# Kernel tuning notes

Measured on AMD Instinct MI355X. Metric: run time of the kernel, lower is better.

Reference implementation:

```python
import jax, jax.numpy as jnp
import numpy as np

NG = 8       # GroupNorm groups
EPS = 1e-5   # torch default eps for GroupNorm/BatchNorm
M_AND = 5    # Anderson history size
MAX_ITER = 25
LAM = 1e-4
BETA = 1.0


def conv2d(x, w):
    # x: [B,C,H,W], w: [O,I,3,3], stride 1, SAME padding (pad=1)
    return jax.lax.conv_general_dilated(x, w, (1, 1), 'SAME',
                                        dimension_numbers=('NCHW', 'OIHW', 'NCHW'))


def group_norm(x, g, b):
    B, C, H, W = x.shape
    xg = x.reshape(B, NG, C // NG, H, W)
    mu = xg.mean((2, 3, 4), keepdims=True)
    var = xg.var((2, 3, 4), keepdims=True)
    xn = ((xg - mu) * jax.lax.rsqrt(var + EPS)).reshape(B, C, H, W)
    return xn * g[None, :, None, None] + b[None, :, None, None]


def batch_norm(x, g, b):
    # training-mode BatchNorm2d: batch statistics over (B,H,W)
    mu = x.mean((0, 2, 3), keepdims=True)
    var = x.var((0, 2, 3), keepdims=True)
    return (x - mu) * jax.lax.rsqrt(var + EPS) * g[None, :, None, None] + b[None, :, None, None]


def resnet_f(p, z, x):
    # y = norm1(relu(conv1(z))); out = norm3(relu(z + norm2(x + conv2(y))))
    y = group_norm(jax.nn.relu(conv2d(z, p['conv1_w'])), p['gn1_g'], p['gn1_b'])
    return group_norm(jax.nn.relu(z + group_norm(x + conv2d(y, p['conv2_w']),
                                                 p['gn2_g'], p['gn2_b'])),
                      p['gn3_g'], p['gn3_b'])


def anderson(f, x0, m=M_AND, lam=LAM, max_iter=MAX_ITER, beta=BETA):
    # Anderson acceleration for fixed point z = f(z); fixed iteration count
    # (the torch version early-exits at tol=0.01; we run the full max_iter for
    # a deterministic jit-friendly reference).
    shape = x0.shape
    bsz = shape[0]
    flat = lambda v: v.reshape(bsz, -1)
    X = [None] * m
    Fv = [None] * m
    X[0] = flat(x0)
    Fv[0] = flat(f(x0))
    X[1] = Fv[0]
    Fv[1] = flat(f(Fv[0].reshape(shape)))
    for k in range(2, max_iter):
        n = min(k, m)
        Xn = jnp.stack(X[:n], 1)   # [B,n,D]
        Fn = jnp.stack(Fv[:n], 1)  # [B,n,D]
        G = Fn - Xn
        Hm = jnp.einsum('bnd,bmd->bnm', G, G) + lam * jnp.eye(n, dtype=x0.dtype)
        Hb = (jnp.zeros((bsz, n + 1, n + 1), x0.dtype)
              .at[:, 1:, 1:].set(Hm)
              .at[:, 0, 1:].set(1.0)
              .at[:, 1:, 0].set(1.0))
        y = jnp.zeros((bsz, n + 1), x0.dtype).at[:, 0].set(1.0)
        alpha = jnp.linalg.solve(Hb, y[..., None])[:, 1:, 0]  # [B,n]
        xk = beta * jnp.einsum('bn,bnd->bd', alpha, Fn) + (1.0 - beta) * jnp.einsum('bn,bnd->bd', alpha, Xn)
        X[k % m] = xk
        Fv[k % m] = flat(f(xk.reshape(shape)))
    return X[(max_iter - 1) % m].reshape(shape)


def setup_inputs() -> dict:
    key = jax.random.key(0)
    ks = jax.random.split(key, 6)
    B, H, W = 8, 128, 200
    f32 = jnp.float32
    return {
        'x': jax.random.normal(ks[0], (B, 1, H, W), f32),
        'conv0_w': jax.random.normal(ks[1], (48, 1, 3, 3), f32) * 0.1,
        'conv0_b': jnp.zeros((48,), f32),
        'bn_g': jnp.ones((48,), f32),
        'bn_b': jnp.zeros((48,), f32),
        'conv1_w': jax.random.normal(ks[2], (64, 48, 3, 3), f32) * 0.01,
        'conv2_w': jax.random.normal(ks[3], (48, 64, 3, 3), f32) * 0.01,
        'gn1_g': jnp.ones((64,), f32), 'gn1_b': jnp.zeros((64,), f32),
        'gn2_g': jnp.ones((48,), f32), 'gn2_b': jnp.zeros((48,), f32),
        'gn3_g': jnp.ones((48,), f32), 'gn3_b': jnp.zeros((48,), f32),
        'fc_w': jax.random.normal(ks[4], (10, 200), f32) * 0.05,
        'fc_b': jnp.zeros((10,), f32),
    }


def reference(x, conv0_w, conv0_b, bn_g, bn_b, conv1_w, conv2_w,
              gn1_g, gn1_b, gn2_g, gn2_b, gn3_g, gn3_b, fc_w, fc_b):
    fp = {'conv1_w': conv1_w, 'conv2_w': conv2_w,
          'gn1_g': gn1_g, 'gn1_b': gn1_b,
          'gn2_g': gn2_g, 'gn2_b': gn2_b,
          'gn3_g': gn3_g, 'gn3_b': gn3_b}
    h = batch_norm(conv2d(x, conv0_w) + conv0_b[None, :, None, None], bn_g, bn_b)
    z_star = anderson(lambda z: resnet_f(fp, z, h), jnp.zeros_like(h))
    z = resnet_f(fp, z_star, h)  # one extra application, as in DEQFixedPoint
    # Linear(200,10) acts on last dim: [B,48,H,200] -> [B,48,H,10]
    return jnp.einsum('bchw,ow->bcho', z, fc_w) + fc_b
```

## Files before the change

kernel.cpp:

```cpp
#include <hip/hip_runtime.h>

#define BB   8
#define HH   128
#define WW   200
#define HWSZ 25600
#define C48  48
#define C64  64
#define NGRP 8
#define EPSV 1e-5f
#define LAMV 1e-4
#define SLOT 9830400
#define DPB  1228800
#define Y64SZ 13107200
#define BIGELEMS 131072000ull

typedef unsigned short bf16_t;
typedef __attribute__((ext_vector_type(4))) short s4v;
typedef __attribute__((ext_vector_type(8))) short s8v;
typedef __attribute__((ext_vector_type(16))) float f32x16;

__device__ inline float b2f(bf16_t b) { return __uint_as_float(((unsigned)b) << 16); }
__device__ inline bf16_t f2b(float f) {
    unsigned u = __float_as_uint(f);
    unsigned r = u + 0x7fffu + ((u >> 16) & 1u);
    return (bf16_t)(r >> 16);
}
__device__ inline float lo16(unsigned u) { return __uint_as_float(u << 16); }
__device__ inline float hi16(unsigned u) { return __uint_as_float(u & 0xffff0000u); }
__device__ inline unsigned pack2(float lo, float hi) {
    return ((unsigned)f2b(lo)) | (((unsigned)f2b(hi)) << 16);
}
__device__ inline float4 ld4(const bf16_t* p) {
    ushort4 u = *(const ushort4*)p;
    return make_float4(b2f(u.x), b2f(u.y), b2f(u.z), b2f(u.w));
}
__device__ inline void st4(bf16_t* p, float4 v) {
    ushort4 u; u.x = f2b(v.x); u.y = f2b(v.y); u.z = f2b(v.z); u.w = f2b(v.w);
    *(ushort4*)p = u;
}
__device__ inline void ld8(const bf16_t* p, float* v) {
    uint4 u = *(const uint4*)p;
    v[0] = lo16(u.x); v[1] = hi16(u.x); v[2] = lo16(u.y); v[3] = hi16(u.y);
    v[4] = lo16(u.z); v[5] = hi16(u.z); v[6] = lo16(u.w); v[7] = hi16(u.w);
}
__device__ inline void st8(bf16_t* p, const float* v) {
    uint4 u;
    u.x = pack2(v[0], v[1]); u.y = pack2(v[2], v[3]);
    u.z = pack2(v[4], v[5]); u.w = pack2(v[6], v[7]);
    *(uint4*)p = u;
}

__device__ inline void ms_from(const double* __restrict__ ds, int pair, double invcnt,
                               float& mean, float& inv) {
    double s = ds[2 * pair], q = ds[2 * pair + 1];
    double m = s * invcnt;
    double v = q * invcnt - m * m;
    mean = (float)m;
    inv = (float)(1.0 / sqrt(v + (double)EPSV));
}


__global__ void zero_kernel(float* __restrict__ p, int n) {
    int i = blockIdx.x * 256 + threadIdx.x;
    if (i < n) p[i] = 0.f;
}
__global__ void fill16_kernel(float4* __restrict__ p) {
    float4 z; z.x = z.y = z.z = z.w = 0.f;
    p[(size_t)blockIdx.x * 256 + threadIdx.x] = z;
}
__global__ void copy16_kernel(float4* __restrict__ dst, const float4* __restrict__ src) {
    size_t i = (size_t)blockIdx.x * 256 + threadIdx.x;
    dst[i] = src[i];
}

__global__ void pack_kernel(const float* __restrict__ w, bf16_t* __restrict__ apk,
                            int CIN, int CO_real, int total) {
    int idx = blockIdx.x * 256 + threadIdx.x;
    if (idx >= total) return;
    int j   = idx & 7;
    int l   = (idx >> 3) & 63;
    int mt  = (idx >> 9) & 1;
    int tap = (idx >> 10) % 9;
    int kc  = idx / 9216;
    int co = mt * 32 + (l & 31);
    int ci = kc * 16 + (l >> 5) * 8 + j;
    float v = (co < CO_real) ? w[((size_t)co * CIN + ci) * 9 + tap] : 0.f;
    apk[idx] = f2b(v);
}

__global__ __launch_bounds__(256) void conv0_kernel(
    const float* __restrict__ x, const float* __restrict__ w0,
    const float* __restrict__ b0, float* __restrict__ out)
{
    __shared__ float xs[3 * 202];
    __shared__ float wt[480];
    const int tid = threadIdx.x;
    const int bI = blockIdx.x / HH, y = blockIdx.x % HH;
    for (int i = tid; i < 606; i += 256) {
        int r = i / 202, cc = i % 202;
        int gy = y + r - 1, gx = cc - 1;
        float v = 0.f;
        if ((unsigned)gy < (unsigned)HH && (unsigned)gx < (unsigned)WW)
            v = x[(size_t)bI * HWSZ + gy * WW + gx];
        xs[r * 202 + cc] = v;
    }
    for (int i = tid; i < 480; i += 256) wt[i] = (i < 432) ? w0[i] : b0[i - 432];
    __syncthreads();
    const size_t obase = (((size_t)bI * HH + y) * WW) * 48;
    for (int ch = tid; ch < 2400; ch += 256) {
        int px = (ch * 4) / 48, c0 = (ch * 4) % 48;
        float xv[3][3];
        #pragma unroll
        for (int r = 0; r < 3; r++)
            #pragma unroll
            for (int dx = 0; dx < 3; dx++)
                xv[r][dx] = xs[r * 202 + px + dx];
        float4 o;
        #pragma unroll
        for (int j = 0; j < 4; j++) {
            int c = c0 + j;
            float acc = wt[432 + c];
            #pragma unroll
            for (int r = 0; r < 3; r++)
                #pragma unroll
                for (int dx = 0; dx < 3; dx++)
                    acc = fmaf(xv[r][dx], wt[c * 9 + r * 3 + dx], acc);
            ((float*)&o)[j] = acc;
        }
        *(float4*)(out + obase + ch * 4) = o;
    }
}

__global__ void bn_stats_kernel(const float* __restrict__ src, double* __restrict__ dst)
{
    __shared__ float ss[192], qq[192];
    const int tid = threadIdx.x;
    const int c = tid % 48, r = tid / 48;
    const int b = blockIdx.y;
    const size_t base = ((size_t)b * HWSZ + (size_t)blockIdx.x * 256) * 48 + c;
    float s = 0.f, q = 0.f;
    for (int p = r; p < 256; p += 4) {
        float v = src[base + (size_t)p * 48];
        s += v; q += v * v;
    }
    ss[tid] = s; qq[tid] = q;
    __syncthreads();
    if (tid < 48) {
        s = ss[tid] + ss[tid + 48] + ss[tid + 96] + ss[tid + 144];
        q = qq[tid] + qq[tid + 48] + qq[tid + 96] + qq[tid + 144];
        unsafeAtomicAdd(&dst[tid * 2],     (double)s);
        unsafeAtomicAdd(&dst[tid * 2 + 1], (double)q);
    }
}

__global__ __launch_bounds__(256) void bn_apply_kernel(
    const float* __restrict__ src, bf16_t* __restrict__ dst,
    const float* __restrict__ gamma, const float* __restrict__ beta,
    const double* __restrict__ ds)
{
    __shared__ float gaT[48], beT[48];
    int tid = threadIdx.x;
    if (tid < 48) {
        float mean, inv; ms_from(ds, tid, 1.0 / 204800.0, mean, inv);
        float ga = gamma[tid] * inv;
        gaT[tid] = ga; beT[tid] = beta[tid] - mean * ga;
    }
    __syncthreads();
    size_t base = (size_t)blockIdx.x * 1024 + (size_t)tid * 4;
    int c0 = (int)(base % 48);
    float4 v = *(const float4*)(src + base);
    ushort4 o;
    o.x = f2b(fmaf(v.x, gaT[c0],     beT[c0]));
    o.y = f2b(fmaf(v.y, gaT[c0 + 1], beT[c0 + 1]));
    o.z = f2b(fmaf(v.z, gaT[c0 + 2], beT[c0 + 2]));
    o.w = f2b(fmaf(v.w, gaT[c0 + 3], beT[c0 + 3]));
    *(ushort4*)(dst + base) = o;
}

template<int CIN, int CIPAD, int CO, int OTS, int CG, bool RELU, bool ADDH, bool FOLDGN>
__global__ __launch_bounds__(256) void conv_mfma_kernel(
    const bf16_t* __restrict__ in, const s8v* __restrict__ apk,
    const bf16_t* __restrict__ hadd, bf16_t* __restrict__ out,
    double* __restrict__ dsOut,
    const double* __restrict__ dsPrev, const float* __restrict__ gPrev,
    const float* __restrict__ bPrev)
{
    constexpr int KC  = CIN / 16;
    constexpr int NCH = CIN / 4;
    const int tid  = threadIdx.x;
    const int lane = tid & 63;
    const int wv   = tid >> 6;
    const int x0 = blockIdx.x * 32;
    const int y0 = blockIdx.y * 4;
    const int b  = blockIdx.z;

    __shared__ __align__(16) bf16_t bt[6 * 34 * CIPAD];
    __shared__ __align__(16) float gaT[FOLDGN ? CIN : 4];
    __shared__ __align__(16) float beT[FOLDGN ? CIN : 4];
    __shared__ float ss[256], qq[256];

    if (FOLDGN) {
        if (tid < CIN) {
            float mean, inv;
            ms_from(dsPrev, b * NGRP + tid / (CIN / NGRP), 1.0 / 204800.0, mean, inv);
            float ga = gPrev[tid] * inv;
            gaT[tid] = ga; beT[tid] = bPrev[tid] - mean * ga;
        }
        __syncthreads();
    }
    for (int i = tid; i < 6 * 34 * NCH; i += 256) {
        int ch = i % NCH, p = i / NCH;
        int r = p / 34, c = p - r * 34;
        int gy = y0 + r - 1, gx = x0 + c - 1;
        ushort4 v = make_ushort4(0, 0, 0, 0);
        if ((unsigned)gy < (unsigned)HH && (unsigned)gx < (unsigned)WW) {
            ushort4 raw = *(const ushort4*)(in + ((((size_t)b * HH + gy) * WW + gx) * CIN + ch * 4));
            if (FOLDGN) {
                float4 ga4 = *(const float4*)&gaT[ch * 4];
                float4 be4 = *(const float4*)&beT[ch * 4];
                v.x = f2b(fmaf(b2f(raw.x), ga4.x, be4.x));
                v.y = f2b(fmaf(b2f(raw.y), ga4.y, be4.y));
                v.z = f2b(fmaf(b2f(raw.z), ga4.z, be4.z));
                v.w = f2b(fmaf(b2f(raw.w), ga4.w, be4.w));
            } else v = raw;
        }
        *(ushort4*)(bt + p * CIPAD + ch * 4) = v;
    }
    __syncthreads();

    const int n = lane & 31, half = lane >> 5;
    f32x16 acc0, acc1;
    #pragma unroll
    for (int i = 0; i < 16; i++) { acc0[i] = 0.f; acc1[i] = 0.f; }

    #pragma unroll
    for (int ky = 0; ky < 3; ky++)
    #pragma unroll
    for (int kx = 0; kx < 3; kx++) {
        const int tap = ky * 3 + kx;
        s8v af[2 * KC];
        #pragma unroll
        for (int kc = 0; kc < KC; kc++) {
            af[2 * kc]     = apk[(size_t)kc * 1152 + tap * 128 + lane];
            af[2 * kc + 1] = apk[(size_t)kc * 1152 + tap * 128 + 64 + lane];
        }
        const bf16_t* brow = bt + ((wv + ky) * 34 + n + kx) * CIPAD + half * 8;
        #pragma unroll
        for (int kc = 0; kc < KC; kc++) {
            s8v bfrag = *(const s8v*)(brow + kc * 16);
            acc0 = __builtin_amdgcn_mfma_f32_32x32x16_bf16(af[2 * kc],     bfrag, acc0, 0, 0, 0);
            acc1 = __builtin_amdgcn_mfma_f32_32x32x16_bf16(af[2 * kc + 1], bfrag, acc1, 0, 0, 0);
        }
    }
    __syncthreads();

    bf16_t* ot = bt;
    {
        const int pxl = wv * 32 + n;
        const bool pv = (x0 + n) < WW;
        #pragma unroll
        for (int g4 = 0; g4 < 4; g4++) {
            s4v pk0;
            #pragma unroll
            for (int jj = 0; jj < 4; jj++) {
                float v = acc0[g4 * 4 + jj];
                if (RELU) v = fmaxf(v, 0.f);
                pk0[jj] = (short)(pv ? f2b(v) : (bf16_t)0);
            }
            *(s4v*)&ot[pxl * OTS + g4 * 8 + 4 * half] = pk0;
            const int c1b = 32 + g4 * 8 + 4 * half;
            if (c1b + 3 < CO) {
                s4v pk1;
                #pragma unroll
                for (int jj = 0; jj < 4; jj++) {
                    float v = acc1[g4 * 4 + jj];
                    if (RELU) v = fmaxf(v, 0.f);
                    pk1[jj] = (short)(pv ? f2b(v) : (bf16_t)0);
                }
                *(s4v*)&ot[pxl * OTS + c1b] = pk1;
            }
        }
    }
    __syncthreads();
    {
        constexpr int NCH8 = 128 * CO / 8;
        for (int ch = tid; ch < NCH8; ch += 256) {
            int pxl = ch / (CO / 8);
            int co0 = (ch % (CO / 8)) * 8;
            int row = pxl >> 5, col = pxl & 31;
            int xx = x0 + col;
            if (xx < WW) {
                bf16_t* lp = &ot[pxl * OTS + co0];
                size_t ga = (((size_t)b * HH + y0 + row) * WW + xx) * CO + co0;
                if (ADDH) {
                    float4 h0 = ld4(hadd + ga), h1 = ld4(hadd + ga + 4);
                    float4 l0 = ld4(lp), l1 = ld4(lp + 4);
                    float4 v0 = make_float4(l0.x + h0.x, l0.y + h0.y, l0.z + h0.z, l0.w + h0.w);
                    float4 v1 = make_float4(l1.x + h1.x, l1.y + h1.y, l1.z + h1.z, l1.w + h1.w);
                    st4(out + ga, v0); st4(out + ga + 4, v1);
                    st4(lp, v0); st4(lp + 4, v1);
                } else {
                    *(ushort4*)(out + ga)     = *(ushort4*)lp;
                    *(ushort4*)(out + ga + 4) = *(ushort4*)(lp + 4);
                }
            }
        }
    }
    if (ADDH) __syncthreads();
    {
        constexpr int NPH = 256 / CO;
        const int c = tid % CO, rr = tid / CO;
        float s = 0.f, q = 0.f;
        if (rr < NPH) {
            for (int px = rr; px < 128; px += NPH) {
                float v = b2f(ot[px * OTS + c]);
                s += v; q += v * v;
            }
        }
        ss[tid] = s; qq[tid] = q;
        __syncthreads();
        if (tid < CO) {
            float S = ss[tid], Q = qq[tid];
            #pragma unroll
            for (int p = 1; p < NPH; p++) { S += ss[tid + p * CO]; Q += qq[tid + p * CO]; }
            ss[tid] = S; qq[tid] = Q;
        }
        __syncthreads();
        if (tid < NGRP) {
            float S = 0.f, Q = 0.f;
            #pragma unroll
            for (int j = 0; j < CG; j++) { S += ss[tid * CG + j]; Q += qq[tid * CG + j]; }
            unsafeAtomicAdd(&dsOut[((size_t)b * NGRP + tid) * 2],     (double)S);
            unsafeAtomicAdd(&dsOut[((size_t)b * NGRP + tid) * 2 + 1], (double)Q);
        }
    }
}

__global__ __launch_bounds__(192) void add_relu_gn2_kernel(
    bf16_t* __restrict__ u, const bf16_t* __restrict__ z,
    const double* __restrict__ ds2, const float* __restrict__ g2,
    const float* __restrict__ b2, double* __restrict__ ds3)
{
    __shared__ float sm[16];
    const int tid = threadIdx.x;
    const int c0 = 8 * (tid % 6), pxr = tid / 6;
    const int b = blockIdx.y;
    if (tid < 16) sm[tid] = 0.f;
    const int gA = c0 / 6;
    const int split = (gA + 1) * 6 - c0;
    float meanA, invA, meanB, invB;
    ms_from(ds2, b * NGRP + gA,     1.0 / 153600.0, meanA, invA);
    ms_from(ds2, b * NGRP + gA + 1, 1.0 / 153600.0, meanB, invB);
    float wga[8], wbe[8];
    #pragma unroll
    for (int e = 0; e < 8; e++) {
        int c = c0 + e;
        float m = (e < split) ? meanA : meanB, iv = (e < split) ? invA : invB;
        float ga = g2[c] * iv;
        wga[e] = ga; wbe[e] = b2[c] - m * ga;
    }
    __syncthreads();
    const size_t pxbase = (size_t)b * HWSZ + (size_t)blockIdx.x * 256;
    float sA = 0.f, qA = 0.f, sB = 0.f, qB = 0.f;
    for (int it = 0; it < 8; it++) {
        size_t idx = (pxbase + it * 32 + pxr) * 48 + c0;
        float uu[8], zz[8], vv[8];
        ld8(u + idx, uu); ld8(z + idx, zz);
        #pragma unroll
        for (int e = 0; e < 8; e++) {
            float v = fmaxf(fmaf(uu[e], wga[e], wbe[e]) + zz[e], 0.f);
            vv[e] = v;
            if (e < split) { sA += v; qA += v * v; } else { sB += v; qB += v * v; }
        }
        st8(u + idx, vv);
    }
    atomicAdd(&sm[2 * gA], sA);     atomicAdd(&sm[2 * gA + 1], qA);
    atomicAdd(&sm[2 * gA + 2], sB); atomicAdd(&sm[2 * gA + 3], qB);
    __syncthreads();
    if (tid < NGRP) {
        unsafeAtomicAdd(&ds3[(b * NGRP + tid) * 2],     (double)sm[tid * 2]);
        unsafeAtomicAdd(&ds3[(b * NGRP + tid) * 2 + 1], (double)sm[tid * 2 + 1]);
    }
}

__global__ __launch_bounds__(192) void gn3_gram_kernel(
    const bf16_t* __restrict__ v, const bf16_t* __restrict__ z,
    bf16_t* __restrict__ F, bf16_t* __restrict__ G,
    const double* __restrict__ ds3, const float* __restrict__ g3,
    const float* __restrict__ b3,
    const bf16_t* __restrict__ Gall, int jslot, int nf, double* __restrict__ gram)
{
    __shared__ double red[3][5];
    const int tid = threadIdx.x;
    const int c0 = 8 * (tid % 6), pxr = tid / 6;
    const int b = blockIdx.y;
    const int gA = c0 / 6;
    const int split = (gA + 1) * 6 - c0;
    float meanA, invA, meanB, invB;
    ms_from(ds3, b * NGRP + gA,     1.0 / 153600.0, meanA, invA);
    ms_from(ds3, b * NGRP + gA + 1, 1.0 / 153600.0, meanB, invB);
    float wga[8], wbe[8];
    #pragma unroll
    for (int e = 0; e < 8; e++) {
        int c = c0 + e;
        float m = (e < split) ? meanA : meanB, iv = (e < split) ? invA : invB;
        float ga = g3[c] * iv;
        wga[e] = ga; wbe[e] = b3[c] - m * ga;
    }
    const size_t pxbase = (size_t)b * HWSZ + (size_t)blockIdx.x * 256;
    double dot[5] = {0.0, 0.0, 0.0, 0.0, 0.0};
    for (int it = 0; it < 8; it++) {
        size_t idx = (pxbase + it * 32 + pxr) * 48 + c0;
        float rr[8];
        ld8(v + idx, rr);
        #pragma unroll
        for (int e = 0; e < 8; e++) rr[e] = fmaf(rr[e], wga[e], wbe[e]);
        st8(F + idx, rr);
        if (nf > 0) {
            float zz[8], gg[8];
            ld8(z + idx, zz);
            #pragma unroll
            for (int e = 0; e < 8; e++) gg[e] = rr[e] - zz[e];
            st8(G + idx, gg);
            #pragma unroll
            for (int i = 0; i < 5; i++) {
                if (i >= nf) continue;
                float d = 0.f;
                if (i == jslot) {
                    #pragma unroll
                    for (int e = 0; e < 8; e++) d = fmaf(gg[e], gg[e], d);
                } else {
                    float gi[8];
                    ld8(Gall + (size_t)i * SLOT + idx, gi);
                    #pragma unroll
                    for (int e = 0; e < 8; e++) d = fmaf(gg[e], gi[e], d);
                }
                dot[i] += (double)d;
            }
        }
    }
    if (nf > 0) {
        #pragma unroll
        for (int i = 0; i < 5; i++) {
            if (i >= nf) continue;
            #pragma unroll
            for (int off = 32; off > 0; off >>= 1) dot[i] += __shfl_down(dot[i], off);
        }
        int wv = tid >> 6;
        if ((tid & 63) == 0) {
            #pragma unroll
            for (int i = 0; i < 5; i++) if (i < nf) red[wv][i] = dot[i];
        }
        __syncthreads();
        if (tid == 0) {
            #pragma unroll
            for (int i = 0; i < 5; i++) {
                if (i >= nf) continue;
                double D = red[0][i] + red[1][i] + red[2][i];
                unsafeAtomicAdd(&gram[b * 25 + jslot * 5 + i], D);
                if (i != jslot) unsafeAtomicAdd(&gram[b * 25 + i * 5 + jslot], D);
            }
        }
    }
}


__global__ void solve_kernel(const double* __restrict__ gram, float* __restrict__ alpha, int n) {
    int b = threadIdx.x;
    if (b >= BB) return;
    const int m = n + 1;
    double A[6][7];
    for (int i = 0; i < m; i++)
        for (int jj = 0; jj <= m; jj++) A[i][jj] = 0.0;
    for (int i = 1; i < m; i++) { A[0][i] = 1.0; A[i][0] = 1.0; }
    for (int i = 1; i < m; i++)
        for (int jj = 1; jj < m; jj++)
            A[i][jj] = gram[b * 25 + (i - 1) * 5 + (jj - 1)] + ((i == jj) ? LAMV : 0.0);
    A[0][m] = 1.0;
    for (int col = 0; col < m; col++) {
        int piv = col; double best = fabs(A[col][col]);
        for (int rr = col + 1; rr < m; rr++) {
            double tv = fabs(A[rr][col]);
            if (tv > best) { best = tv; piv = rr; }
        }
        if (piv != col)
            for (int cc = col; cc <= m; cc++) {
                double tmp = A[col][cc]; A[col][cc] = A[piv][cc]; A[piv][cc] = tmp;
            }
        double invp = 1.0 / A[col][col];
        for (int cc = col; cc <= m; cc++) A[col][cc] *= invp;
        for (int rr = 0; rr < m; rr++) {
            if (rr == col) continue;
            double f = A[rr][col];
            if (f != 0.0)
                for (int cc = col; cc <= m; cc++) A[rr][cc] = fma(-f, A[col][cc], A[rr][cc]);
        }
    }
    for (int i = 0; i < n; i++) alpha[b * 5 + i] = (float)A[i + 1][m];
}

__global__ __launch_bounds__(256) void xk_kernel(
    const bf16_t* __restrict__ Fb, const float* __restrict__ alpha,
    bf16_t* __restrict__ zcur, int n, double* __restrict__ gram, int jz, int nf)
{
    if (blockIdx.x == 0 && threadIdx.x < 8 * nf) {
        int b = threadIdx.x / nf, i = threadIdx.x % nf;
        gram[b * 25 + jz * 5 + i] = 0.0;
        gram[b * 25 + i * 5 + jz] = 0.0;
    }
    const int b = blockIdx.x / 75;
    float al[5];
    #pragma unroll
    for (int j = 0; j < 5; j++) al[j] = (j < n) ? alpha[b * 5 + j] : 0.f;
    const size_t base = (size_t)blockIdx.x * 16384 + (size_t)threadIdx.x * 8;
    for (int it = 0; it < 8; it++) {
        size_t idx = base + (size_t)it * 2048;
        float s[8] = {0.f, 0.f, 0.f, 0.f, 0.f, 0.f, 0.f, 0.f};
        #pragma unroll
        for (int j = 0; j < 5; j++) {
            if (j < n) {
                float f[8];
                ld8(Fb + (size_t)j * SLOT + idx, f);
                #pragma unroll
                for (int e = 0; e < 8; e++) s[e] = fmaf(f[e], al[j], s[e]);
            }
        }
        st8(zcur + idx, s);
    }
}

__global__ __launch_bounds__(512) void fc_kernel(
    const bf16_t* __restrict__ zf, const float* __restrict__ fw,
    const float* __restrict__ fb, float* __restrict__ out)
{
    __shared__ bf16_t row[9600];
    __shared__ float fwT[2000];
    int tid = threadIdx.x;
    int b = blockIdx.x >> 7, hh = blockIdx.x & 127;
    size_t base = (((size_t)b * HH + hh) * WW) * 48;
    for (int i = tid; i < 2400; i += 512)
        *(ushort4*)&row[i * 4] = *(const ushort4*)(zf + base + (size_t)i * 4);
    for (int i = tid; i < 2000; i += 512) fwT[i] = fw[i];
    __syncthreads();
    if (tid < 480) {
        int c = tid % 48, o = tid / 48;
        float acc = fb[o];
        #pragma unroll 4
        for (int w = 0; w < 200; w++)
            acc = fmaf(b2f(row[w * 48 + c]), fwT[o * 200 + w], acc);
        out[(((size_t)b * 48 + c) * HH + hh) * 10 + o] = acc;
    }
}


static inline int imin(int a, int b) { return a < b ? a : b; }

extern "C" void kernel_launch(void* const* d_in, const int* in_sizes, int n_in,
                              void* d_out, int out_size, void* d_ws, size_t ws_size,
                              hipStream_t stream)
{
    const float* x   = (const float*)d_in[0];
    const float* w0  = (const float*)d_in[1];
    const float* b0  = (const float*)d_in[2];
    const float* bng = (const float*)d_in[3];
    const float* bnb = (const float*)d_in[4];
    const float* w1  = (const float*)d_in[5];
    const float* w2  = (const float*)d_in[6];
    const float* g1  = (const float*)d_in[7];
    const float* be1 = (const float*)d_in[8];
    const float* g2  = (const float*)d_in[9];
    const float* be2 = (const float*)d_in[10];
    const float* g3  = (const float*)d_in[11];
    const float* be3 = (const float*)d_in[12];
    const float* fcw = (const float*)d_in[13];
    const float* fcb = (const float*)d_in[14];
    float* out = (float*)d_out;

    bf16_t* h    = (bf16_t*)d_ws;
    bf16_t* zcur = h + (size_t)SLOT;
    bf16_t* y64  = zcur + (size_t)SLOT;
    bf16_t* Fb   = y64 + (size_t)Y64SZ;
    bf16_t* Gb   = Fb + 5 * (size_t)SLOT;
    double* dstats = (double*)((char*)d_ws + BIGELEMS * 2);
    double* gram   = dstats + 9696;
    float*  alpha  = (float*)(gram + 200);
    bf16_t* apk1   = (bf16_t*)(alpha + 40);
    bf16_t* apk2   = apk1 + 27648;
    float*  scratch = (float*)Gb;

    const size_t need = BIGELEMS * 2 + 9696 * 8 + 200 * 8 + 40 * 4 + (27648 + 36864) * 2;
    if (ws_size < need) return;

    const dim3 blk(256);
    const int CHUNKS16 = SLOT * 2 / 16 / 256;

    zero_kernel<<<(19792 + 255) / 256, blk, 0, stream>>>((float*)dstats, 19792);
    pack_kernel<<<108, blk, 0, stream>>>(w1, apk1, 48, 64, 27648);
    pack_kernel<<<144, blk, 0, stream>>>(w2, apk2, 64, 48, 36864);
    fill16_kernel<<<CHUNKS16, blk, 0, stream>>>((float4*)zcur);

    conv0_kernel<<<BB * HH, blk, 0, stream>>>(x, w0, b0, scratch);
    bn_stats_kernel<<<dim3(100, BB), dim3(192), 0, stream>>>(scratch, dstats);
    bn_apply_kernel<<<SLOT / 1024, blk, 0, stream>>>(scratch, h, bng, bnb, dstats);

    int call = 0;
    auto resnet = [&](const bf16_t* zin, bf16_t* Fdst, bf16_t* Gdst, int jslot, int nf) {
        double* ds = dstats + 96 + 384 * call;
        call++;
        dim3 cg(7, 32, BB);
        conv_mfma_kernel<48, 56, 64, 66, 8, true, false, false><<<cg, blk, 0, stream>>>(
            zin, (const s8v*)apk1, nullptr, y64, ds, nullptr, nullptr, nullptr);
        conv_mfma_kernel<64, 72, 48, 50, 6, false, true, true><<<cg, blk, 0, stream>>>(
            y64, (const s8v*)apk2, h, Fdst, ds + 128, ds, g1, be1);
        add_relu_gn2_kernel<<<dim3(100, BB), dim3(192), 0, stream>>>(
            Fdst, zin, ds + 128, g2, be2, ds + 256);
        gn3_gram_kernel<<<dim3(100, BB), dim3(192), 0, stream>>>(
            Fdst, zin, Fdst, Gdst, ds + 256, g3, be3, Gb, jslot, nf, gram);
    };

    resnet(zcur, Fb, Gb, 0, 1);
    copy16_kernel<<<CHUNKS16, blk, 0, stream>>>((float4*)zcur, (const float4*)Fb);
    resnet(zcur, Fb + (size_t)SLOT, Gb + (size_t)SLOT, 1, 2);

    for (int k = 2; k <= 24; k++) {
        int n = imin(k, 5);
        int j = k % 5;
        int nf = imin(k + 1, 5);
        solve_kernel<<<1, 64, 0, stream>>>(gram, alpha, n);
        xk_kernel<<<600, blk, 0, stream>>>(Fb, alpha, zcur, n, gram, j, nf);
        if (k < 24)
            resnet(zcur, Fb + (size_t)j * SLOT, Gb + (size_t)j * SLOT, j, nf);
    }

    resnet(zcur, Fb, nullptr, 0, 0);

    fc_kernel<<<BB * HH, dim3(512), 0, stream>>>(Fb, fcw, fcb, out);
}
```

Measured before the change: 5.214 ms.

## Process two row tiles per conv block with prefetched halo rows

Each conv block now computes 8 output rows in two 4-row passes instead of one 4-row tile, so the grid is halved. The 2-row halo between the passes is reused from shared memory. Global loads for the second pass's new rows are issued before the first pass's MFMA loop and written to LDS afterwards, overlapping the loads with compute. The input staging also switches to 16-byte chunks. In exchange, shared-memory use and register pressure rise (a separate output tile, prefetch registers), occupancy may drop, and the grid has fewer blocks.

After: 5.937 ms. +13.9%, slower.

```diff
diff --git a/kernel.cpp b/kernel.cpp
--- a/kernel.cpp
+++ b/kernel.cpp
@@ -186,15 +186,19 @@
     const float* __restrict__ bPrev)
 {
     constexpr int KC  = CIN / 16;
-    constexpr int NCH = CIN / 4;
+    constexpr int NCK = CIN / 8;
+    constexpr int RCH = 34 * NCK;
+    constexpr int ST0 = (6 * RCH + 255) / 256;
+    constexpr int PRE = (4 * RCH + 255) / 256;
     const int tid  = threadIdx.x;
     const int lane = tid & 63;
     const int wv   = tid >> 6;
     const int x0 = blockIdx.x * 32;
-    const int y0 = blockIdx.y * 4;
+    const int yg = blockIdx.y * 8;
     const int b  = blockIdx.z;
 
-    __shared__ __align__(16) bf16_t bt[6 * 34 * CIPAD];
+    __shared__ __align__(16) bf16_t buf[10 * 34 * CIPAD];
+    __shared__ __align__(16) bf16_t ot[128 * OTS];
     __shared__ __align__(16) float gaT[FOLDGN ? CIN : 4];
     __shared__ __align__(16) float beT[FOLDGN ? CIN : 4];
     __shared__ float ss[256], qq[256];
@@ -208,131 +212,186 @@
         }
         __syncthreads();
     }
-    for (int i = tid; i < 6 * 34 * NCH; i += 256) {
-        int ch = i % NCH, p = i / NCH;
-        int r = p / 34, c = p - r * 34;
-        int gy = y0 + r - 1, gx = x0 + c - 1;
-        ushort4 v = make_ushort4(0, 0, 0, 0);
-        if ((unsigned)gy < (unsigned)HH && (unsigned)gx < (unsigned)WW) {
-            ushort4 raw = *(const ushort4*)(in + ((((size_t)b * HH + gy) * WW + gx) * CIN + ch * 4));
-            if (FOLDGN) {
-                float4 ga4 = *(const float4*)&gaT[ch * 4];
-                float4 be4 = *(const float4*)&beT[ch * 4];
-                v.x = f2b(fmaf(b2f(raw.x), ga4.x, be4.x));
-                v.y = f2b(fmaf(b2f(raw.y), ga4.y, be4.y));
-                v.z = f2b(fmaf(b2f(raw.z), ga4.z, be4.z));
-                v.w = f2b(fmaf(b2f(raw.w), ga4.w, be4.w));
-            } else v = raw;
-        }
-        *(ushort4*)(bt + p * CIPAD + ch * 4) = v;
+
+    auto loadChunk = [&](int gy, int px, int chk) -> uint4 {
+        uint4 r = make_uint4(0, 0, 0, 0);
+        int gx = x0 - 1 + px;
+        if ((unsigned)gy < (unsigned)HH && (unsigned)gx < (unsigned)WW)
+            r = *(const uint4*)(in + (((size_t)b * HH + gy) * WW + gx) * CIN + chk * 8);
+        return r;
+    };
+    auto writeChunk = [&](int L, int px, int chk, uint4 raw) {
+        bf16_t* dst = buf + ((L * 34 + px) * CIPAD) + chk * 8;
+        int gy = yg - 1 + L, gx = x0 - 1 + px;
+        bool valid = ((unsigned)gy < (unsigned)HH) && ((unsigned)gx < (unsigned)WW);
+        if (!valid) {
+            uint4 z = make_uint4(0, 0, 0, 0);
+            *(uint4*)dst = z;
+            return;
+        }
+        if (FOLDGN) {
+            float v[8];
+            v[0] = lo16(raw.x); v[1] = hi16(raw.x); v[2] = lo16(raw.y); v[3] = hi16(raw.y);
+            v[4] = lo16(raw.z); v[5] = hi16(raw.z); v[6] = lo16(raw.w); v[7] = hi16(raw.w);
+            int c0 = chk * 8;
+            #pragma unroll
+            for (int e = 0; e < 8; e++) v[e] = fmaf(v[e], gaT[c0 + e], beT[c0 + e]);
+            st8(dst, v);
+        } else {
+            *(uint4*)dst = raw;
+        }
+    };
+
+    {
+        uint4 sbuf[ST0];
+        #pragma unroll
+        for (int j = 0; j < ST0; j++) {
+            int idx = tid + j * 256;
+            if (idx < 6 * RCH) {
+                int L = idx / RCH, rem = idx - L * RCH;
+                sbuf[j] = loadChunk(yg - 1 + L, rem / NCK, rem % NCK);
+            }
+        }
+        #pragma unroll
+        for (int j = 0; j < ST0; j++) {
+            int idx = tid + j * 256;
+            if (idx < 6 * RCH) {
+                int L = idx / RCH, rem = idx - L * RCH;
+                writeChunk(L, rem / NCK, rem % NCK, sbuf[j]);
+            }
+        }
     }
     __syncthreads();
 
     const int n = lane & 31, half = lane >> 5;
-    f32x16 acc0, acc1;
-    #pragma unroll
-    for (int i = 0; i < 16; i++) { acc0[i] = 0.f; acc1[i] = 0.f; }
-
-    #pragma unroll
-    for (int ky = 0; ky < 3; ky++)
-    #pragma unroll
-    for (int kx = 0; kx < 3; kx++) {
-        const int tap = ky * 3 + kx;
-        s8v af[2 * KC];
-        #pragma unroll
-        for (int kc = 0; kc < KC; kc++) {
-            af[2 * kc]     = apk[(size_t)kc * 1152 + tap * 128 + lane];
-            af[2 * kc + 1] = apk[(size_t)kc * 1152 + tap * 128 + 64 + lane];
-        }
-        const bf16_t* brow = bt + ((wv + ky) * 34 + n + kx) * CIPAD + half * 8;
-        #pragma unroll
-        for (int kc = 0; kc < KC; kc++) {
-            s8v bfrag = *(const s8v*)(brow + kc * 16);
-            acc0 = __builtin_amdgcn_mfma_f32_32x32x16_bf16(af[2 * kc],     bfrag, acc0, 0, 0, 0);
-            acc1 = __builtin_amdgcn_mfma_f32_32x32x16_bf16(af[2 * kc + 1], bfrag, acc1, 0, 0, 0);
-        }
-    }
-    __syncthreads();
-
-    bf16_t* ot = bt;
-    {
-        const int pxl = wv * 32 + n;
-        const bool pv = (x0 + n) < WW;
-        #pragma unroll
-        for (int g4 = 0; g4 < 4; g4++) {
-            s4v pk0;
-            #pragma unroll
-            for (int jj = 0; jj < 4; jj++) {
-                float v = acc0[g4 * 4 + jj];
-                if (RELU) v = fmaxf(v, 0.f);
-                pk0[jj] = (short)(pv ? f2b(v) : (bf16_t)0);
-            }
-            *(s4v*)&ot[pxl * OTS + g4 * 8 + 4 * half] = pk0;
-            const int c1b = 32 + g4 * 8 + 4 * half;
-            if (c1b + 3 < CO) {
-                s4v pk1;
+
+    for (int t = 0; t < 2; t++) {
+        const int y0t = yg + 4 * t;
+        uint4 pbuf[PRE];
+        if (t == 0) {
+            #pragma unroll
+            for (int j = 0; j < PRE; j++) {
+                int idx = tid + j * 256;
+                if (idx < 4 * RCH) {
+                    int rl = idx / RCH, rem = idx - rl * RCH;
+                    pbuf[j] = loadChunk(yg + 5 + rl, rem / NCK, rem % NCK);
+                }
+            }
+        }
+        f32x16 acc0, acc1;
+        #pragma unroll
+        for (int i = 0; i < 16; i++) { acc0[i] = 0.f; acc1[i] = 0.f; }
+        #pragma unroll
+        for (int ky = 0; ky < 3; ky++) {
+            const int Lrow = 4 * t + wv + ky;
+            #pragma unroll
+            for (int kx = 0; kx < 3; kx++) {
+                const int tap = ky * 3 + kx;
+                s8v af[2 * KC];
+                #pragma unroll
+                for (int kc = 0; kc < KC; kc++) {
+                    af[2 * kc]     = apk[(size_t)kc * 1152 + tap * 128 + lane];
+                    af[2 * kc + 1] = apk[(size_t)kc * 1152 + tap * 128 + 64 + lane];
+                }
+                const bf16_t* brow = buf + (Lrow * 34 + n + kx) * CIPAD + half * 8;
+                #pragma unroll
+                for (int kc = 0; kc < KC; kc++) {
+                    s8v bfrag = *(const s8v*)(brow + kc * 16);
+                    acc0 = __builtin_amdgcn_mfma_f32_32x32x16_bf16(af[2 * kc],     bfrag, acc0, 0, 0, 0);
+                    acc1 = __builtin_amdgcn_mfma_f32_32x32x16_bf16(af[2 * kc + 1], bfrag, acc1, 0, 0, 0);
+                }
+            }
+        }
+        if (t == 0) {
+            #pragma unroll
+            for (int j = 0; j < PRE; j++) {
+                int idx = tid + j * 256;
+                if (idx < 4 * RCH) {
+                    int rl = idx / RCH, rem = idx - rl * RCH;
+                    writeChunk(6 + rl, rem / NCK, rem % NCK, pbuf[j]);
+                }
+            }
+        }
+        {
+            const int pxl = wv * 32 + n;
+            const bool pv = (x0 + n) < WW;
+            #pragma unroll
+            for (int g4 = 0; g4 < 4; g4++) {
+                s4v pk0;
                 #pragma unroll
                 for (int jj = 0; jj < 4; jj++) {
-                    float v = acc1[g4 * 4 + jj];
+                    float v = acc0[g4 * 4 + jj];
                     if (RELU) v = fmaxf(v, 0.f);
-                    pk1[jj] = (short)(pv ? f2b(v) : (bf16_t)0);
-                }
-                *(s4v*)&ot[pxl * OTS + c1b] = pk1;
-            }
-        }
-    }
-    __syncthreads();
-    {
-        constexpr int NCH8 = 128 * CO / 8;
-        for (int ch = tid; ch < NCH8; ch += 256) {
-            int pxl = ch / (CO / 8);
-            int co0 = (ch % (CO / 8)) * 8;
-            int row = pxl >> 5, col = pxl & 31;
-            int xx = x0 + col;
-            if (xx < WW) {
-                bf16_t* lp = &ot[pxl * OTS + co0];
-                size_t ga = (((size_t)b * HH + y0 + row) * WW + xx) * CO + co0;
-                if (ADDH) {
-                    float4 h0 = ld4(hadd + ga), h1 = ld4(hadd + ga + 4);
-                    float4 l0 = ld4(lp), l1 = ld4(lp + 4);
-                    float4 v0 = make_float4(l0.x + h0.x, l0.y + h0.y, l0.z + h0.z, l0.w + h0.w);
-                    float4 v1 = make_float4(l1.x + h1.x, l1.y + h1.y, l1.z + h1.z, l1.w + h1.w);
-                    st4(out + ga, v0); st4(out + ga + 4, v1);
-                    st4(lp, v0); st4(lp + 4, v1);
-                } else {
-                    *(ushort4*)(out + ga)     = *(ushort4*)lp;
-                    *(ushort4*)(out + ga + 4) = *(ushort4*)(lp + 4);
-                }
-            }
-        }
-    }
-    if (ADDH) __syncthreads();
-    {
-        constexpr int NPH = 256 / CO;
-        const int c = tid % CO, rr = tid / CO;
-        float s = 0.f, q = 0.f;
-        if (rr < NPH) {
-            for (int px = rr; px < 128; px += NPH) {
-                float v = b2f(ot[px * OTS + c]);
-                s += v; q += v * v;
-            }
-        }
-        ss[tid] = s; qq[tid] = q;
+                    pk0[jj] = (short)(pv ? f2b(v) : (bf16_t)0);
+                }
+                *(s4v*)&ot[pxl * OTS + g4 * 8 + 4 * half] = pk0;
+                const int c1b = 32 + g4 * 8 + 4 * half;
+                if (c1b + 3 < CO) {
+                    s4v pk1;
+                    #pragma unroll
+                    for (int jj = 0; jj < 4; jj++) {
+                        float v = acc1[g4 * 4 + jj];
+                        if (RELU) v = fmaxf(v, 0.f);
+                        pk1[jj] = (short)(pv ? f2b(v) : (bf16_t)0);
+                    }
+                    *(s4v*)&ot[pxl * OTS + c1b] = pk1;
+                }
+            }
+        }
         __syncthreads();
-        if (tid < CO) {
-            float S = ss[tid], Q = qq[tid];
-            #pragma unroll
-            for (int p = 1; p < NPH; p++) { S += ss[tid + p * CO]; Q += qq[tid + p * CO]; }
-            ss[tid] = S; qq[tid] = Q;
+        {
+            constexpr int NCH8 = 128 * CO / 8;
+            for (int ch = tid; ch < NCH8; ch += 256) {
+                int pxl = ch / (CO / 8);
+                int co0 = (ch % (CO / 8)) * 8;
+                int row = pxl >> 5, col = pxl & 31;
+                int xx = x0 + col;
+                if (xx < WW) {
+                    bf16_t* lp = &ot[pxl * OTS + co0];
+                    size_t ga = (((size_t)b * HH + y0t + row) * WW + xx) * CO + co0;
+                    if (ADDH) {
+                        float4 h0 = ld4(hadd + ga), h1 = ld4(hadd + ga + 4);
+                        float4 l0 = ld4(lp), l1 = ld4(lp + 4);
+                        float4 v0 = make_float4(l0.x + h0.x, l0.y + h0.y, l0.z + h0.z, l0.w + h0.w);
+                        float4 v1 = make_float4(l1.x + h1.x, l1.y + h1.y, l1.z + h1.z, l1.w + h1.w);
+                        st4(out + ga, v0); st4(out + ga + 4, v1);
+                        st4(lp, v0); st4(lp + 4, v1);
+                    } else {
+                        *(ushort4*)(out + ga)     = *(ushort4*)lp;
+                        *(ushort4*)(out + ga + 4) = *(ushort4*)(lp + 4);
+                    }
+                }
+            }
         }
         __syncthreads();
-        if (tid < NGRP) {
-            float S = 0.f, Q = 0.f;
-            #pragma unroll
-            for (int j = 0; j < CG; j++) { S += ss[tid * CG + j]; Q += qq[tid * CG + j]; }
-            unsafeAtomicAdd(&dsOut[((size_t)b * NGRP + tid) * 2],     (double)S);
-            unsafeAtomicAdd(&dsOut[((size_t)b * NGRP + tid) * 2 + 1], (double)Q);
-        }
+        {
+            constexpr int NPH = 256 / CO;
+            const int c = tid % CO, rr = tid / CO;
+            float s = 0.f, q = 0.f;
+            if (rr < NPH) {
+                for (int px = rr; px < 128; px += NPH) {
+                    float v = b2f(ot[px * OTS + c]);
+                    s += v; q += v * v;
+                }
+            }
+            ss[tid] = s; qq[tid] = q;
+            __syncthreads();
+            if (tid < CO) {
+                float S = ss[tid], Q = qq[tid];
+                #pragma unroll
+                for (int p = 1; p < NPH; p++) { S += ss[tid + p * CO]; Q += qq[tid + p * CO]; }
+                ss[tid] = S; qq[tid] = Q;
+            }
+            __syncthreads();
+            if (tid < NGRP) {
+                float S = 0.f, Q = 0.f;
+                #pragma unroll
+                for (int j = 0; j < CG; j++) { S += ss[tid * CG + j]; Q += qq[tid * CG + j]; }
+                unsafeAtomicAdd(&dsOut[((size_t)b * NGRP + tid) * 2],     (double)S);
+                unsafeAtomicAdd(&dsOut[((size_t)b * NGRP + tid) * 2 + 1], (double)Q);
+            }
+        }
+        __syncthreads();
     }
 }
 
@@ -607,7 +666,7 @@
     auto resnet = [&](const bf16_t* zin, bf16_t* Fdst, bf16_t* Gdst, int jslot, int nf) {
         double* ds = dstats + 96 + 384 * call;
         call++;
-        dim3 cg(7, 32, BB);
+        dim3 cg(7, 16, BB);
         conv_mfma_kernel<48, 56, 64, 66, 8, true, false, false><<<cg, blk, 0, stream>>>(
             zin, (const s8v*)apk1, nullptr, y64, ds, nullptr, nullptr, nullptr);
         conv_mfma_kernel<64, 72, 48, 50, 6, false, true, true><<<cg, blk, 0, stream>>>(
```
